# Performance work log

Hardware: AMD Instinct MI355X
Metric: run time of the kernel (lower is better)

The kernel has to match this reference:

```python
import jax, jax.numpy as jnp
import numpy as np

OUT_DIM = 4096
DPC = 16
N = OUT_DIM * DPC  # 65536
BATCH = 512


def setup_inputs() -> dict:
    key = jax.random.key(0)
    k1, k2 = jax.random.split(key)
    x = jax.random.normal(k1, (BATCH, N), dtype=jnp.float32)
    duty_cycle = jax.random.uniform(k2, (N,), dtype=jnp.float32)
    boost_strength = jnp.ones((1,), dtype=jnp.float32)
    return {"x": x, "duty_cycle": duty_cycle, "boost_strength": boost_strength}


def reference(x, duty_cycle, boost_strength):
    # GenericKWinners.forward in training mode (k = out_dim), boost_strength > 0.
    n = x.shape[1]
    target_density = OUT_DIM / n
    bs = boost_strength[0]
    boost_factors = jnp.exp((target_density - duty_cycle) * bs)  # [N]
    # x is detached in the original before boosting/masking
    boosted = jax.lax.stop_gradient(x) * boost_factors  # [B, N]
    # Overlapping windows: group k covers [k*(dpc-1), k*(dpc-1)+dpc)
    starts = jnp.arange(OUT_DIM) * (DPC - 1)  # [OUT_DIM]
    win_idx = starts[:, None] + jnp.arange(DPC)[None, :]  # [OUT_DIM, DPC]
    windows = boosted[:, win_idx]  # [B, OUT_DIM, DPC]
    ind = jnp.argmax(windows, axis=-1)  # [B, OUT_DIM]
    mask = jax.nn.one_hot(ind, DPC, dtype=x.dtype)  # [B, OUT_DIM, DPC]
    mask = mask.reshape(x.shape[0], OUT_DIM * DPC)  # [B, N]
    return mask * x
```

## Files before the change

kernel.cpp:

```cpp
#include <hip/hip_runtime.h>

#define OUT_DIM 4096
#define DPC     16
#define NCOL    65536
#define BATCH   512

typedef float nvec4 __attribute__((ext_vector_type(4)));

__global__ void boost_table_kernel(const float* __restrict__ duty,
                                   const float* __restrict__ bs_ptr,
                                   float* __restrict__ bf) {
    int p = blockIdx.x * blockDim.x + threadIdx.x;
    if (p < NCOL) {
        float t = (0.0625f - duty[p]) * bs_ptr[0];
        bf[p] = (float)exp((double)t);
    }
}

__global__ __launch_bounds__(512, 4) void dkw_kernel(const float* __restrict__ x,
                                                     const float* __restrict__ bf,
                                                     float* __restrict__ out) {
    __shared__ float sb[16384];
    __shared__ unsigned char sjb[1024];

    const int tid = threadIdx.x;
    const int r   = blockIdx.x >> 2;
    const int b   = blockIdx.x & 3;
    const int rowbase = r << 16;
    const int span_f  = b * 15360;

    const float4* __restrict__ xg4 = (const float4*)(x + rowbase + span_f);
    const float4* __restrict__ bg4 = (const float4*)(bf + span_f);
    float4* sb4 = (float4*)sb;
    #pragma unroll
    for (int k = 0; k < 8; ++k) {
        const int i = tid + (k << 9);
        float4 a = xg4[i];
        float4 c = bg4[i];
        a.x *= c.x; a.y *= c.y; a.z *= c.z; a.w *= c.w;
        sb4[i] = a;
    }
    __syncthreads();

    const float4* __restrict__ xo_g = (const float4*)(x + rowbase + (b << 14));
    float4 xo[8];
    #pragma unroll
    for (int k = 0; k < 8; ++k)
        xo[k] = xo_g[tid + (k << 9)];

    #pragma unroll
    for (int m = 0; m < 2; ++m) {
        const int w = tid + (m << 9);
        const float* __restrict__ p = sb + w * 15;
        float best = p[0];
        int   bj   = 0;
        #pragma unroll
        for (int kk = 1; kk < DPC; ++kk) {
            float v = p[kk];
            if (v > best) { best = v; bj = kk; }
        }
        sjb[w] = (unsigned char)bj;
    }
    __syncthreads();

    float4* __restrict__ og4 = (float4*)(out + rowbase + (b << 14));
    #pragma unroll
    for (int k = 0; k < 8; ++k) {
        const int o4 = tid + (k << 9);
        const int jm = (int)sjb[o4 >> 2];
        const int j0 = (o4 & 3) << 2;
        const float4 v = xo[k];
        float4 o;
        o.x = (j0     == jm) ? v.x : 0.0f;
        o.y = (j0 + 1 == jm) ? v.y : 0.0f;
        o.z = (j0 + 2 == jm) ? v.z : 0.0f;
        o.w = (j0 + 3 == jm) ? v.w : 0.0f;
        __builtin_nontemporal_store(*(const nvec4*)&o, (nvec4*)&og4[o4]);
    }
}

extern "C" void kernel_launch(void* const* d_in, const int* in_sizes, int n_in,
                              void* d_out, int out_size, void* d_ws, size_t ws_size,
                              hipStream_t stream) {
    const float* x    = (const float*)d_in[0];
    const float* duty = (const float*)d_in[1];
    const float* bs   = (const float*)d_in[2];
    float* out = (float*)d_out;
    float* bf  = (float*)d_ws;

    hipLaunchKernelGGL(boost_table_kernel, dim3(NCOL / 256), dim3(256), 0, stream,
                       duty, bs, bf);
    hipLaunchKernelGGL(dkw_kernel, dim3(BATCH * 4), dim3(512), 0, stream,
                       x, bf, out);
}
```

Measured before the change: 243.8 us.

## Make the windowed argmax kernel persistent with register prefetch of the next chunk

The kernel becomes persistent: 1024 blocks of 256 threads loop over 4096 half-size chunks (8 per row). While each block runs the argmax and masked store for the current chunk, it loads the x and boost slices for its next chunk into registers, so global load latency overlaps with compute and stores. Barriers are replaced by an LDS-only waitcnt plus s_barrier, which lets those outstanding global loads stay in flight across the barrier. The cost is higher register pressure from the prefetch buffers and a smaller per-chunk working set.

```diff
diff --git a/kernel.cpp b/kernel.cpp
--- a/kernel.cpp
+++ b/kernel.cpp
@@ -4,6 +4,9 @@
 #define DPC     16
 #define NCOL    65536
 #define BATCH   512
+#define NCHUNK  4096
+#define NBLK    1024
+#define ITERS   (NCHUNK / NBLK)
 
 typedef float nvec4 __attribute__((ext_vector_type(4)));
 
@@ -17,65 +20,93 @@
     }
 }
 
-__global__ __launch_bounds__(512, 4) void dkw_kernel(const float* __restrict__ x,
+__device__ __forceinline__ void lds_barrier() {
+    asm volatile("s_waitcnt lgkmcnt(0)" ::: "memory");
+    __builtin_amdgcn_s_barrier();
+}
+
+__global__ __launch_bounds__(256, 4) void dkw_kernel(const float* __restrict__ x,
                                                      const float* __restrict__ bf,
                                                      float* __restrict__ out) {
-    __shared__ float sb[16384];
-    __shared__ unsigned char sjb[1024];
+    __shared__ float sb[8192];
+    __shared__ unsigned char sjb[512];
 
     const int tid = threadIdx.x;
-    const int r   = blockIdx.x >> 2;
-    const int b   = blockIdx.x & 3;
-    const int rowbase = r << 16;
-    const int span_f  = b * 15360;
+    int c = blockIdx.x;
 
-    const float4* __restrict__ xg4 = (const float4*)(x + rowbase + span_f);
-    const float4* __restrict__ bg4 = (const float4*)(bf + span_f);
+    float4 xn[8], bn[8];
+    {
+        const int r = c >> 3, h = c & 7;
+        const float4* __restrict__ xg = (const float4*)(x + (r << 16) + h * 7680);
+        const float4* __restrict__ bg = (const float4*)(bf + h * 7680);
+        #pragma unroll
+        for (int k = 0; k < 8; ++k) {
+            xn[k] = xg[tid + (k << 8)];
+            bn[k] = bg[tid + (k << 8)];
+        }
+    }
+
     float4* sb4 = (float4*)sb;
-    #pragma unroll
-    for (int k = 0; k < 8; ++k) {
-        const int i = tid + (k << 9);
-        float4 a = xg4[i];
-        float4 c = bg4[i];
-        a.x *= c.x; a.y *= c.y; a.z *= c.z; a.w *= c.w;
-        sb4[i] = a;
-    }
-    __syncthreads();
+    #pragma unroll 1
+    for (int it = 0; it < ITERS; ++it) {
+        const int r = c >> 3, h = c & 7;
 
-    const float4* __restrict__ xo_g = (const float4*)(x + rowbase + (b << 14));
-    float4 xo[8];
-    #pragma unroll
-    for (int k = 0; k < 8; ++k)
-        xo[k] = xo_g[tid + (k << 9)];
+        #pragma unroll
+        for (int k = 0; k < 8; ++k) {
+            float4 a = xn[k], bq = bn[k];
+            a.x *= bq.x; a.y *= bq.y; a.z *= bq.z; a.w *= bq.w;
+            sb4[tid + (k << 8)] = a;
+        }
+        lds_barrier();
 
-    #pragma unroll
-    for (int m = 0; m < 2; ++m) {
-        const int w = tid + (m << 9);
-        const float* __restrict__ p = sb + w * 15;
-        float best = p[0];
-        int   bj   = 0;
+        const float4* __restrict__ xo_g = (const float4*)(x + (r << 16) + (h << 13));
+        float4 xo[8];
         #pragma unroll
-        for (int kk = 1; kk < DPC; ++kk) {
-            float v = p[kk];
-            if (v > best) { best = v; bj = kk; }
+        for (int k = 0; k < 8; ++k)
+            xo[k] = xo_g[tid + (k << 8)];
+
+        const int cn = c + NBLK;
+        if (cn < NCHUNK) {
+            const int rn = cn >> 3, hn = cn & 7;
+            const float4* __restrict__ xg = (const float4*)(x + (rn << 16) + hn * 7680);
+            const float4* __restrict__ bg = (const float4*)(bf + hn * 7680);
+            #pragma unroll
+            for (int k = 0; k < 8; ++k) {
+                xn[k] = xg[tid + (k << 8)];
+                bn[k] = bg[tid + (k << 8)];
+            }
         }
-        sjb[w] = (unsigned char)bj;
-    }
-    __syncthreads();
 
-    float4* __restrict__ og4 = (float4*)(out + rowbase + (b << 14));
-    #pragma unroll
-    for (int k = 0; k < 8; ++k) {
-        const int o4 = tid + (k << 9);
-        const int jm = (int)sjb[o4 >> 2];
-        const int j0 = (o4 & 3) << 2;
-        const float4 v = xo[k];
-        float4 o;
-        o.x = (j0     == jm) ? v.x : 0.0f;
-        o.y = (j0 + 1 == jm) ? v.y : 0.0f;
-        o.z = (j0 + 2 == jm) ? v.z : 0.0f;
-        o.w = (j0 + 3 == jm) ? v.w : 0.0f;
-        __builtin_nontemporal_store(*(const nvec4*)&o, (nvec4*)&og4[o4]);
+        #pragma unroll
+        for (int m = 0; m < 2; ++m) {
+            const int w = tid + (m << 8);
+            const float* __restrict__ p = sb + w * 15;
+            float best = p[0];
+            int   bj   = 0;
+            #pragma unroll
+            for (int kk = 1; kk < DPC; ++kk) {
+                float v = p[kk];
+                if (v > best) { best = v; bj = kk; }
+            }
+            sjb[w] = (unsigned char)bj;
+        }
+        lds_barrier();
+
+        float4* __restrict__ og4 = (float4*)(out + (r << 16) + (h << 13));
+        #pragma unroll
+        for (int k = 0; k < 8; ++k) {
+            const int o4 = tid + (k << 8);
+            const int jm = (int)sjb[o4 >> 2];
+            const int j0 = (o4 & 3) << 2;
+            const float4 v = xo[k];
+            float4 o;
+            o.x = (j0     == jm) ? v.x : 0.0f;
+            o.y = (j0 + 1 == jm) ? v.y : 0.0f;
+            o.z = (j0 + 2 == jm) ? v.z : 0.0f;
+            o.w = (j0 + 3 == jm) ? v.w : 0.0f;
+            __builtin_nontemporal_store(*(const nvec4*)&o, (nvec4*)&og4[o4]);
+        }
+        c = cn;
     }
 }
 
@@ -90,6 +121,6 @@
 
     hipLaunchKernelGGL(boost_table_kernel, dim3(NCOL / 256), dim3(256), 0, stream,
                        duty, bs, bf);
-    hipLaunchKernelGGL(dkw_kernel, dim3(BATCH * 4), dim3(512), 0, stream,
+    hipLaunchKernelGGL(dkw_kernel, dim3(NBLK), dim3(256), 0, stream,
                        x, bf, out);
 }
```

After: 246.2 us. No clear change (+1.0%).

## Split rows into eight chunks and reuse window loads for output

Applied to the files above, without the earlier changes.

Each row is now split into eight blocks covering 512 windows each instead of four blocks of 1024. Each block loads one contiguous x span into registers once and reuses it both for the boosted shared-memory window scan and for the masked output, where the old code read the x span and the output span separately. Halving shared memory per block allows higher occupancy (launch bounds 8), and a lighter barrier that only waits on LDS replaces __syncthreads. In exchange there are more guarded loads, predication in the store loop, and some threads whose loaded x is discarded.

```diff
diff --git a/kernel.cpp b/kernel.cpp
--- a/kernel.cpp
+++ b/kernel.cpp
@@ -4,6 +4,7 @@
 #define DPC     16
 #define NCOL    65536
 #define BATCH   512
+#define NCHUNK  4096
 
 typedef float nvec4 __attribute__((ext_vector_type(4)));
 
@@ -17,41 +18,47 @@
     }
 }
 
-__global__ __launch_bounds__(512, 4) void dkw_kernel(const float* __restrict__ x,
+__device__ __forceinline__ void lds_barrier() {
+    asm volatile("s_waitcnt lgkmcnt(0)" ::: "memory");
+    __builtin_amdgcn_s_barrier();
+}
+
+__global__ __launch_bounds__(512, 8) void dkw_kernel(const float* __restrict__ x,
                                                      const float* __restrict__ bf,
                                                      float* __restrict__ out) {
-    __shared__ float sb[16384];
-    __shared__ unsigned char sjb[1024];
+    __shared__ float sb[7696];
+    __shared__ unsigned char sjb[512];
 
     const int tid = threadIdx.x;
-    const int r   = blockIdx.x >> 2;
-    const int b   = blockIdx.x & 3;
-    const int rowbase = r << 16;
-    const int span_f  = b * 15360;
+    const int r   = blockIdx.x >> 3;
+    const int h   = blockIdx.x & 7;
+    const int U   = 2048 + (h << 7);
+    const int off = h << 7;
 
-    const float4* __restrict__ xg4 = (const float4*)(x + rowbase + span_f);
-    const float4* __restrict__ bg4 = (const float4*)(bf + span_f);
+    const float4* __restrict__ xg4 = (const float4*)x + (r << 14) + 1920 * h;
+    const float4* __restrict__ bg4 = (const float4*)bf + 1920 * h;
     float4* sb4 = (float4*)sb;
+
+    float4 xn[6];
     #pragma unroll
-    for (int k = 0; k < 8; ++k) {
+    for (int k = 0; k < 6; ++k) {
         const int i = tid + (k << 9);
-        float4 a = xg4[i];
-        float4 c = bg4[i];
-        a.x *= c.x; a.y *= c.y; a.z *= c.z; a.w *= c.w;
-        sb4[i] = a;
+        if (i < U) xn[k] = xg4[i];
     }
-    __syncthreads();
+    #pragma unroll
+    for (int k = 0; k < 4; ++k) {
+        const int i = tid + (k << 9);
+        if (i < 1924) {
+            float4 a = xn[k];
+            float4 q = bg4[i];
+            a.x *= q.x; a.y *= q.y; a.z *= q.z; a.w *= q.w;
+            sb4[i] = a;
+        }
+    }
+    lds_barrier();
 
-    const float4* __restrict__ xo_g = (const float4*)(x + rowbase + (b << 14));
-    float4 xo[8];
-    #pragma unroll
-    for (int k = 0; k < 8; ++k)
-        xo[k] = xo_g[tid + (k << 9)];
-
-    #pragma unroll
-    for (int m = 0; m < 2; ++m) {
-        const int w = tid + (m << 9);
-        const float* __restrict__ p = sb + w * 15;
+    {
+        const float* __restrict__ p = sb + tid * 15;
         float best = p[0];
         int   bj   = 0;
         #pragma unroll
@@ -59,23 +66,26 @@
             float v = p[kk];
             if (v > best) { best = v; bj = kk; }
         }
-        sjb[w] = (unsigned char)bj;
+        sjb[tid] = (unsigned char)bj;
     }
-    __syncthreads();
+    lds_barrier();
 
-    float4* __restrict__ og4 = (float4*)(out + rowbase + (b << 14));
+    float4* __restrict__ og4 = (float4*)out + (r << 14) + (h << 11);
     #pragma unroll
-    for (int k = 0; k < 8; ++k) {
-        const int o4 = tid + (k << 9);
-        const int jm = (int)sjb[o4 >> 2];
-        const int j0 = (o4 & 3) << 2;
-        const float4 v = xo[k];
-        float4 o;
-        o.x = (j0     == jm) ? v.x : 0.0f;
-        o.y = (j0 + 1 == jm) ? v.y : 0.0f;
-        o.z = (j0 + 2 == jm) ? v.z : 0.0f;
-        o.w = (j0 + 3 == jm) ? v.w : 0.0f;
-        __builtin_nontemporal_store(*(const nvec4*)&o, (nvec4*)&og4[o4]);
+    for (int k = 0; k < 6; ++k) {
+        const int i = tid + (k << 9);
+        if (i >= off && i < U) {
+            const int j  = i - off;
+            const int jm = (int)sjb[j >> 2];
+            const int j0 = (j & 3) << 2;
+            const float4 v = xn[k];
+            float4 o;
+            o.x = (j0     == jm) ? v.x : 0.0f;
+            o.y = (j0 + 1 == jm) ? v.y : 0.0f;
+            o.z = (j0 + 2 == jm) ? v.z : 0.0f;
+            o.w = (j0 + 3 == jm) ? v.w : 0.0f;
+            __builtin_nontemporal_store(*(const nvec4*)&o, (nvec4*)&og4[j]);
+        }
     }
 }
 
@@ -90,6 +100,6 @@
 
     hipLaunchKernelGGL(boost_table_kernel, dim3(NCOL / 256), dim3(256), 0, stream,
                        duty, bs, bf);
-    hipLaunchKernelGGL(dkw_kernel, dim3(BATCH * 4), dim3(512), 0, stream,
+    hipLaunchKernelGGL(dkw_kernel, dim3(NCHUNK), dim3(512), 0, stream,
                        x, bf, out);
 }
```

Measured after the change: 242.0 us. Within noise of the previous version (-0.7%).
